# Kernel tuning notes

Measured on AMD Instinct MI355X. Metric: run time of the kernel, lower is better.

Reference implementation:

```python
import jax, jax.numpy as jnp
import numpy as np
import math

N_PTS = 262144
STEP_LENGTH = math.sqrt(3.0) / 1024.0  # step_length = sqrt(3)/steps


def pos_enc(x):
    # classic NeRF frequency encoding: identity + sin/cos at 10 octaves -> 3 + 3*2*10 = 63
    freqs = 2.0 ** jnp.arange(10, dtype=x.dtype)            # [10]
    xb = x[..., :, None] * freqs                            # [N,3,10]
    xb = xb.reshape(x.shape[0], -1)                         # [N,30]
    return jnp.concatenate([x, jnp.sin(xb), jnp.cos(xb)], axis=-1)  # [N,63]


def dir_enc(u):
    # 26-dim frequency encoding of (dir+1)/2 (color head input 283 = 256 + 26 + 1).
    # 13 sin/cos pairs: per-channel octaves 2^0..2^4, truncated to 13 frequencies.
    freqs = 2.0 ** jnp.arange(5, dtype=u.dtype)             # [5]
    z = (u[..., :, None] * freqs).reshape(u.shape[0], -1)[:, :13]  # [N,13]
    return jnp.concatenate([jnp.sin(z), jnp.cos(z)], axis=-1)      # [N,26]


def linear(x, w, b):
    return x @ w.T + b


def setup_inputs() -> dict:
    key = jax.random.key(0)
    ks = jax.random.split(key, 16)
    s = 0.05
    inp = {
        "position": jax.random.uniform(ks[0], (N_PTS, 3), dtype=jnp.float32),
        "direction": jax.random.uniform(ks[1], (N_PTS, 3), dtype=jnp.float32, minval=-1.0, maxval=1.0),
        "w1_in": jax.random.normal(ks[2], (256, 63), jnp.float32) * s,
        "b1_in": jnp.zeros((256,), jnp.float32),
        "w1_h": jax.random.normal(ks[3], (3, 256, 256), jnp.float32) * s,
        "b1_h": jnp.zeros((3, 256), jnp.float32),
        "w2_in": jax.random.normal(ks[4], (256, 319), jnp.float32) * s,
        "b2_in": jnp.zeros((256,), jnp.float32),
        "w2_h": jax.random.normal(ks[5], (3, 256, 256), jnp.float32) * s,
        "b2_h": jnp.zeros((3, 256), jnp.float32),
        # sigma head Linear(256,1)
        "w_sigma": jax.random.normal(ks[6], (1, 256), jnp.float32) * s,
        "b_sigma": jnp.zeros((1,), jnp.float32),
        # color head Linear(283,128) -> ReLU -> Linear(128,3)
        "w_c1": jax.random.normal(ks[7], (128, 283), jnp.float32) * s,
        "b_c1": jnp.zeros((128,), jnp.float32),
        "w_c2": jax.random.normal(ks[8], (3, 128), jnp.float32) * s,
        "b_c2": jnp.zeros((3,), jnp.float32),
    }
    return inp


def reference(position, direction,
              w1_in, b1_in, w1_h, b1_h,
              w2_in, b2_in, w2_h, b2_h,
              w_sigma, b_sigma, w_c1, b_c1, w_c2, b_c2):
    pe = pos_enc(position)                                  # [N,63]
    h = jax.nn.relu(linear(pe, w1_in, b1_in))               # [N,256]
    for i in range(3):
        h = jax.nn.relu(linear(h, w1_h[i], b1_h[i]))
    g = jax.nn.relu(linear(jnp.concatenate([h, pe], axis=-1), w2_in, b2_in))  # [N,256]
    for i in range(3):
        g = jax.nn.relu(linear(g, w2_h[i], b2_h[i]))
    sigma_raw = linear(g, w_sigma, b_sigma)                 # [N,1]
    # get_alpha: 1 - exp(-relu(sigma) * step_length)
    alphas = 1.0 - jnp.exp(-jax.nn.relu(sigma_raw) * STEP_LENGTH)             # [N,1]
    # get_rgb: shares base features; concat [256 | 26 | 1] = 283
    de = dir_enc((direction + 1.0) * 0.5)                   # [N,26]
    feats = jnp.concatenate([g, de, sigma_raw], axis=-1)    # [N,283]
    rgb = jax.nn.sigmoid(linear(jax.nn.relu(linear(feats, w_c1, b_c1)), w_c2, b_c2))  # [N,3]
    return (rgb, alphas)
```

## Files before the change

kernel.cpp:

```cpp
#include <hip/hip_runtime.h>
#include <hip/hip_bf16.h>

#define N_PTS 262144
#define STEP_LEN 0.0016914558667664818f

using f32x4 = __attribute__((ext_vector_type(4))) float;
using s8 = __attribute__((ext_vector_type(8))) short;

__device__ __forceinline__ float bf2f(short s) {
    union { unsigned int u; float f; } v;
    v.u = ((unsigned int)(unsigned short)s) << 16;
    return v.f;
}
__device__ __forceinline__ short f2bf(float f) {
    __hip_bfloat16 h = __float2bfloat16(f);
    return *reinterpret_cast<short*>(&h);
}

#define OFF_W1    0
#define OFF_L1H0  16384
#define OFF_W2    212992
#define OFF_L2H0  294912
#define OFF_C1G   491520
#define OFF_C1DE  524288
#define OFF_WSIG  528384
#define OFF_WC2   528640
#define WS_ELEMS  532480

__device__ __forceinline__ float hid_val(const float* __restrict__ W, int e) {
    int j = e & 7, lane = (e >> 3) & 63, nt = (e >> 9) & 15, ks = e >> 13;
    int n = nt * 16 + (lane & 15), hi = lane >> 4;
    int f = ks * 32 + ((j >> 2) << 4) + hi * 4 + (j & 3);
    return W[n * 256 + f];
}

__global__ void prep_weights(const float* __restrict__ w1_in,
                             const float* __restrict__ w1_h,
                             const float* __restrict__ w2_in,
                             const float* __restrict__ w2_h,
                             const float* __restrict__ w_c1,
                             const float* __restrict__ w_sigma,
                             const float* __restrict__ w_c2,
                             __hip_bfloat16* __restrict__ ws) {
    int i = blockIdx.x * blockDim.x + threadIdx.x;
    if (i >= WS_ELEMS) return;
    float v;
    if (i < OFF_L1H0) {
        int e = i;
        int j = e & 7, lane = (e >> 3) & 63, nt = (e >> 9) & 15, ks = e >> 13;
        int n = nt * 16 + (lane & 15), hi = lane >> 4;
        int f = ks * 32 + hi * 8 + j;
        v = (f < 63) ? w1_in[n * 63 + f] : 0.f;
    } else if (i < OFF_W2) {
        int e = i - OFF_L1H0; int sub = e >> 16; e &= 65535;
        v = hid_val(w1_h + sub * 65536, e);
    } else if (i < OFF_L2H0) {
        int e = i - OFF_W2;
        int j = e & 7, lane = (e >> 3) & 63, nt = (e >> 9) & 15, ks = e >> 13;
        int n = nt * 16 + (lane & 15), hi = lane >> 4;
        if (ks < 8) {
            int f = ks * 32 + ((j >> 2) << 4) + hi * 4 + (j & 3);
            v = w2_in[n * 319 + f];
        } else {
            int pf = (ks - 8) * 32 + hi * 8 + j;
            v = (pf < 63) ? w2_in[n * 319 + 256 + pf] : 0.f;
        }
    } else if (i < OFF_C1G) {
        int e = i - OFF_L2H0; int sub = e >> 16; e &= 65535;
        v = hid_val(w2_h + sub * 65536, e);
    } else if (i < OFF_C1DE) {
        int e = i - OFF_C1G;
        int j = e & 7, lane = (e >> 3) & 63, nt = (e >> 9) & 7, ks = e >> 12;
        int n = nt * 16 + (lane & 15), hi = lane >> 4;
        int f = ks * 32 + ((j >> 2) << 4) + hi * 4 + (j & 3);
        v = w_c1[n * 283 + f];
    } else if (i < OFF_WSIG) {
        int e = i - OFF_C1DE;
        int j = e & 7, lane = (e >> 3) & 63, nt = (e >> 9) & 7;
        int n = nt * 16 + (lane & 15), hi = lane >> 4;
        int k = 256 + hi * 8 + j;
        v = (k < 283) ? w_c1[n * 283 + k] : 0.f;
    } else if (i < OFF_WC2) {
        int e = i - OFF_WSIG;
        int j = e & 7, hi = (e >> 3) & 3, ks = e >> 5;
        int f = ks * 32 + ((j >> 2) << 4) + hi * 4 + (j & 3);
        v = w_sigma[f];
    } else if (i < 529024) {
        int e = i - OFF_WC2;
        int j = e & 7, hi = (e >> 3) & 3, ks = (e >> 5) & 3, ch = e >> 7;
        int f = ks * 32 + ((j >> 2) << 4) + hi * 4 + (j & 3);
        v = w_c2[ch * 128 + f];
    } else {
        v = 0.f;
    }
    ws[i] = __float2bfloat16(v);
}

__device__ __forceinline__ float enc3(int f, float x0, float x1, float x2) {
    if (f < 3) return (f == 0) ? x0 : ((f == 1) ? x1 : x2);
    if (f < 33) {
        int q = f - 3; int c = q / 10, o = q % 10;
        float xc = (c == 0) ? x0 : ((c == 1) ? x1 : x2);
        return __sinf(xc * (float)(1 << o));
    }
    if (f < 63) {
        int q = f - 33; int c = q / 10, o = q % 10;
        float xc = (c == 0) ? x0 : ((c == 1) ? x1 : x2);
        return __cosf(xc * (float)(1 << o));
    }
    return 0.f;
}

#define MFMA16 __builtin_amdgcn_mfma_f32_16x16x32_bf16

#define GLL(SRC, DST) __builtin_amdgcn_global_load_lds( \
    (const unsigned int*)(SRC), (unsigned int*)(DST), 16, 0, 0)

#define STAGE8(BYTEOFF, DBUF) do { \
    const char* _src = wsB + (long)(BYTEOFF) + wid * 8192 + lane * 16; \
    char* _dst = (DBUF) + wid * 8192; \
    GLL(_src,        _dst);        GLL(_src + 1024, _dst + 1024); \
    GLL(_src + 2048, _dst + 2048); GLL(_src + 3072, _dst + 3072); \
    GLL(_src + 4096, _dst + 4096); GLL(_src + 5120, _dst + 5120); \
    GLL(_src + 6144, _dst + 6144); GLL(_src + 7168, _dst + 7168); \
} while (0)

#define WHALF(RD, SUB, A0, A1, FIRSTV) do { \
    _Pragma("unroll") \
    for (int nt = 0; nt < 16; ++nt) { \
        const s8 w = *(const s8*)((RD) + (SUB) + nt * 1024 + lane * 16); \
        acc[nt][0] = MFMA16(w, (A0), (FIRSTV) ? Z : acc[nt][0], 0, 0, 0); \
        acc[nt][1] = MFMA16(w, (A1), (FIRSTV) ? Z : acc[nt][1], 0, 0, 0); \
    } } while (0)

#define CHALF(RD, SUB, A0, A1, FIRSTV) do { \
    _Pragma("unroll") \
    for (int nt = 0; nt < 8; ++nt) { \
        const s8 w = *(const s8*)((RD) + (SUB) + nt * 1024 + lane * 16); \
        acc[nt][0] = MFMA16(w, (A0), (FIRSTV) ? Z : acc[nt][0], 0, 0, 0); \
        acc[nt][1] = MFMA16(w, (A1), (FIRSTV) ? Z : acc[nt][1], 0, 0, 0); \
    } } while (0)

#define PBAR do { asm volatile("s_waitcnt vmcnt(0)" ::: "memory"); \
                  __builtin_amdgcn_s_barrier(); } while (0)

#define CONVERTL(BOFF) do { \
    _Pragma("unroll") \
    for (int nt = 0; nt < 16; ++nt) { \
        const f32x4 b4 = *(const f32x4*)(biasL + (((BOFF) + nt * 16 + hi4) << 2)); \
        _Pragma("unroll") \
        for (int r = 0; r < 4; ++r) { \
            actA[nt >> 1][((nt & 1) << 2) | r] = f2bf(fmaxf(acc[nt][0][r] + b4[r], 0.f)); \
            actB[nt >> 1][((nt & 1) << 2) | r] = f2bf(fmaxf(acc[nt][1][r] + b4[r], 0.f)); \
        } } } while (0)

#define LAYER4_ODD(CB, BO) do { \
    STAGE8((CB) +  32768, B0); __builtin_amdgcn_s_setprio(1); \
    WHALF(B1, 0, actA[0], actB[0], 1); WHALF(B1, 16384, actA[1], actB[1], 0); \
    __builtin_amdgcn_s_setprio(0); PBAR; \
    STAGE8((CB) +  65536, B1); __builtin_amdgcn_s_setprio(1); \
    WHALF(B0, 0, actA[2], actB[2], 0); WHALF(B0, 16384, actA[3], actB[3], 0); \
    __builtin_amdgcn_s_setprio(0); PBAR; \
    STAGE8((CB) +  98304, B0); __builtin_amdgcn_s_setprio(1); \
    WHALF(B1, 0, actA[4], actB[4], 0); WHALF(B1, 16384, actA[5], actB[5], 0); \
    __builtin_amdgcn_s_setprio(0); PBAR; \
    STAGE8((CB) + 131072, B1); __builtin_amdgcn_s_setprio(1); \
    WHALF(B0, 0, actA[6], actB[6], 0); WHALF(B0, 16384, actA[7], actB[7], 0); \
    __builtin_amdgcn_s_setprio(0); CONVERTL(BO); PBAR; \
} while (0)

#define LAYER4_EVEN(CB, BO) do { \
    STAGE8((CB) +  32768, B1); __builtin_amdgcn_s_setprio(1); \
    WHALF(B0, 0, actA[0], actB[0], 1); WHALF(B0, 16384, actA[1], actB[1], 0); \
    __builtin_amdgcn_s_setprio(0); PBAR; \
    STAGE8((CB) +  65536, B0); __builtin_amdgcn_s_setprio(1); \
    WHALF(B1, 0, actA[2], actB[2], 0); WHALF(B1, 16384, actA[3], actB[3], 0); \
    __builtin_amdgcn_s_setprio(0); PBAR; \
    STAGE8((CB) +  98304, B1); __builtin_amdgcn_s_setprio(1); \
    WHALF(B0, 0, actA[4], actB[4], 0); WHALF(B0, 16384, actA[5], actB[5], 0); \
    __builtin_amdgcn_s_setprio(0); PBAR; \
    STAGE8((CB) + 131072, B0); __builtin_amdgcn_s_setprio(1); \
    WHALF(B1, 0, actA[6], actB[6], 0); WHALF(B1, 16384, actA[7], actB[7], 0); \
    __builtin_amdgcn_s_setprio(0); CONVERTL(BO); PBAR; \
} while (0)

__global__ __launch_bounds__(256, 2) void nerf_fused(
    const float* __restrict__ pos, const float* __restrict__ dir,
    const __hip_bfloat16* __restrict__ ws,
    const float* __restrict__ b1_in, const float* __restrict__ b1_h,
    const float* __restrict__ b2_in, const float* __restrict__ b2_h,
    const float* __restrict__ b_sigma, const float* __restrict__ b_c1,
    const float* __restrict__ b_c2,
    float* __restrict__ out) {

    __shared__ __align__(16) char Lds[74240];
    char* const B0 = Lds;
    char* const B1 = Lds + 32768;
    char* const biasL = Lds + 65536;

    const int t = threadIdx.x;
    const int lane = t & 63;
    const int wid = t >> 6;
    const int hi = lane >> 4;
    const int col = lane & 15;
    const int hi4 = hi * 4;
    const int row0 = blockIdx.x * 128;
    const int gA = row0 + wid * 32 + col;
    const int gB = gA + 16;
    const char* wsB = (const char*)ws;

    STAGE8(0L, B0);

    for (int i = t; i < 2176; i += 256) {
        float v;
        if (i < 256) v = b1_in[i];
        else if (i < 1024) v = b1_h[i - 256];
        else if (i < 1280) v = b2_in[i - 1024];
        else if (i < 2048) v = b2_h[i - 1280];
        else v = b_c1[i - 2048];
        *(float*)(biasL + i * 4) = v;
    }

    s8 peA0, peA1, peB0, peB1;
    {
        float xa0 = pos[gA*3], xa1 = pos[gA*3+1], xa2 = pos[gA*3+2];
        float xb0 = pos[gB*3], xb1 = pos[gB*3+1], xb2 = pos[gB*3+2];
#pragma unroll
        for (int j = 0; j < 8; ++j) {
            int f0 = hi * 8 + j, f1 = 32 + hi * 8 + j;
            peA0[j] = f2bf(enc3(f0, xa0, xa1, xa2));
            peA1[j] = f2bf(enc3(f1, xa0, xa1, xa2));
            peB0[j] = f2bf(enc3(f0, xb0, xb1, xb2));
            peB1[j] = f2bf(enc3(f1, xb0, xb1, xb2));
        }
    }

    s8 deA, deB;
    {
        float uA0 = (dir[gA*3+0] + 1.f) * 0.5f;
        float uA1 = (dir[gA*3+1] + 1.f) * 0.5f;
        float uA2 = (dir[gA*3+2] + 1.f) * 0.5f;
        float uB0 = (dir[gB*3+0] + 1.f) * 0.5f;
        float uB1 = (dir[gB*3+1] + 1.f) * 0.5f;
        float uB2 = (dir[gB*3+2] + 1.f) * 0.5f;
#pragma unroll
        for (int j = 0; j < 8; ++j) {
            int d = hi * 8 + j;
            float vA = 0.f, vB = 0.f;
            if (d < 13) {
                int c = d / 5, o = d % 5; float s = (float)(1 << o);
                vA = __sinf(((c == 0) ? uA0 : (c == 1) ? uA1 : uA2) * s);
                vB = __sinf(((c == 0) ? uB0 : (c == 1) ? uB1 : uB2) * s);
            } else if (d < 26) {
                int q = d - 13; int c = q / 5, o = q % 5; float s = (float)(1 << o);
                vA = __cosf(((c == 0) ? uA0 : (c == 1) ? uA1 : uA2) * s);
                vB = __cosf(((c == 0) ? uB0 : (c == 1) ? uB1 : uB2) * s);
            }
            deA[j] = f2bf(vA); deB[j] = f2bf(vB);
        }
    }

    f32x4 acc[16][2];
    s8 actA[8], actB[8];
    const f32x4 Z = {0.f, 0.f, 0.f, 0.f};

    asm volatile("s_waitcnt vmcnt(0) lgkmcnt(0)" ::: "memory");
    __builtin_amdgcn_s_barrier();

    STAGE8(1L*32768, B1);
    __builtin_amdgcn_s_setprio(1);
    WHALF(B0, 0, peA0, peB0, 1); WHALF(B0, 16384, peA1, peB1, 0);
    __builtin_amdgcn_s_setprio(0);
    CONVERTL(0); PBAR;

#pragma unroll 1
    for (int l = 0; l < 3; ++l)
        LAYER4_ODD(32768L + (long)l * 131072, 256 + (l << 8));

    STAGE8(14L*32768, B0);
    __builtin_amdgcn_s_setprio(1);
    WHALF(B1, 0, actA[0], actB[0], 1); WHALF(B1, 16384, actA[1], actB[1], 0);
    __builtin_amdgcn_s_setprio(0); PBAR;
    STAGE8(15L*32768, B1);
    __builtin_amdgcn_s_setprio(1);
    WHALF(B0, 0, actA[2], actB[2], 0); WHALF(B0, 16384, actA[3], actB[3], 0);
    __builtin_amdgcn_s_setprio(0); PBAR;
    STAGE8(16L*32768, B0);
    __builtin_amdgcn_s_setprio(1);
    WHALF(B1, 0, actA[4], actB[4], 0); WHALF(B1, 16384, actA[5], actB[5], 0);
    __builtin_amdgcn_s_setprio(0); PBAR;
    STAGE8(17L*32768, B1);
    __builtin_amdgcn_s_setprio(1);
    WHALF(B0, 0, actA[6], actB[6], 0); WHALF(B0, 16384, actA[7], actB[7], 0);
    __builtin_amdgcn_s_setprio(0); PBAR;
    STAGE8(18L*32768, B0);
    __builtin_amdgcn_s_setprio(1);
    WHALF(B1, 0, peA0, peB0, 0); WHALF(B1, 16384, peA1, peB1, 0);
    __builtin_amdgcn_s_setprio(0);
    CONVERTL(1024); PBAR;

#pragma unroll 1
    for (int l = 0; l < 3; ++l)
        LAYER4_EVEN(589824L + (long)l * 131072, 1280 + (l << 8));

    float srA, srB, alphaA, alphaB;
    {
        float sA = 0.f, sB = 0.f;
#pragma unroll
        for (int ks = 0; ks < 8; ++ks) {
            const s8 wv = *(const s8*)(wsB + (OFF_WSIG + ks * 32 + hi * 8) * 2);
#pragma unroll
            for (int j = 0; j < 8; ++j) {
                sA += bf2f(actA[ks][j]) * bf2f(wv[j]);
                sB += bf2f(actB[ks][j]) * bf2f(wv[j]);
            }
        }
        sA += __shfl_xor(sA, 16); sA += __shfl_xor(sA, 32);
        sB += __shfl_xor(sB, 16); sB += __shfl_xor(sB, 32);
        srA = sA + b_sigma[0]; srB = sB + b_sigma[0];
        alphaA = 1.f - __expf(-fmaxf(srA, 0.f) * STEP_LEN);
        alphaB = 1.f - __expf(-fmaxf(srB, 0.f) * STEP_LEN);
        if (hi == 3) { deA[2] = f2bf(srA); deB[2] = f2bf(srB); }
    }

    STAGE8(31L*32768, B1);
    __builtin_amdgcn_s_setprio(1);
    CHALF(B0, 0,     actA[0], actB[0], 1);
    CHALF(B0, 8192,  actA[1], actB[1], 0);
    CHALF(B0, 16384, actA[2], actB[2], 0);
    CHALF(B0, 24576, actA[3], actB[3], 0);
    __builtin_amdgcn_s_setprio(0); PBAR;

    {
        const char* _src = wsB + 1048576L + wid * 2048 + lane * 16;
        char* _dst = B0 + wid * 2048;
        GLL(_src, _dst); GLL(_src + 1024, _dst + 1024);
    }
    __builtin_amdgcn_s_setprio(1);
    CHALF(B1, 0,     actA[4], actB[4], 0);
    CHALF(B1, 8192,  actA[5], actB[5], 0);
    CHALF(B1, 16384, actA[6], actB[6], 0);
    CHALF(B1, 24576, actA[7], actB[7], 0);
    __builtin_amdgcn_s_setprio(0); PBAR;

    __builtin_amdgcn_s_setprio(1);
#pragma unroll
    for (int nt = 0; nt < 8; ++nt) {
        const s8 w = *(const s8*)(B0 + nt * 1024 + lane * 16);
        acc[nt][0] = MFMA16(w, deA, acc[nt][0], 0, 0, 0);
        acc[nt][1] = MFMA16(w, deB, acc[nt][1], 0, 0, 0);
    }
    __builtin_amdgcn_s_setprio(0);

    s8 c1A[4], c1B[4];
#pragma unroll
    for (int nt = 0; nt < 8; ++nt) {
        const f32x4 b4 = *(const f32x4*)(biasL + ((2048 + nt * 16 + hi4) << 2));
#pragma unroll
        for (int r = 0; r < 4; ++r) {
            c1A[nt >> 1][((nt & 1) << 2) | r] = f2bf(fmaxf(acc[nt][0][r] + b4[r], 0.f));
            c1B[nt >> 1][((nt & 1) << 2) | r] = f2bf(fmaxf(acc[nt][1][r] + b4[r], 0.f));
        }
    }

#pragma unroll
    for (int ch = 0; ch < 3; ++ch) {
        float rA = 0.f, rB = 0.f;
#pragma unroll
        for (int ks = 0; ks < 4; ++ks) {
            const s8 wv = *(const s8*)(wsB + (OFF_WC2 + (ch * 4 + ks) * 32 + hi * 8) * 2);
#pragma unroll
            for (int j = 0; j < 8; ++j) {
                rA += bf2f(c1A[ks][j]) * bf2f(wv[j]);
                rB += bf2f(c1B[ks][j]) * bf2f(wv[j]);
            }
        }
        rA += __shfl_xor(rA, 16); rA += __shfl_xor(rA, 32);
        rB += __shfl_xor(rB, 16); rB += __shfl_xor(rB, 32);
        if (hi == 0) {
            out[gA * 3 + ch] = 1.f / (1.f + __expf(-(rA + b_c2[ch])));
            out[gB * 3 + ch] = 1.f / (1.f + __expf(-(rB + b_c2[ch])));
        }
    }
    if (hi == 0) {
        out[3 * N_PTS + gA] = alphaA;
        out[3 * N_PTS + gB] = alphaB;
    }
}

extern "C" void kernel_launch(void* const* d_in, const int* in_sizes, int n_in,
                              void* d_out, int out_size, void* d_ws, size_t ws_size,
                              hipStream_t stream) {
    const float* position = (const float*)d_in[0];
    const float* direction = (const float*)d_in[1];
    const float* w1_in = (const float*)d_in[2];
    const float* b1_in = (const float*)d_in[3];
    const float* w1_h  = (const float*)d_in[4];
    const float* b1_h  = (const float*)d_in[5];
    const float* w2_in = (const float*)d_in[6];
    const float* b2_in = (const float*)d_in[7];
    const float* w2_h  = (const float*)d_in[8];
    const float* b2_h  = (const float*)d_in[9];
    const float* w_sigma = (const float*)d_in[10];
    const float* b_sigma = (const float*)d_in[11];
    const float* w_c1  = (const float*)d_in[12];
    const float* b_c1  = (const float*)d_in[13];
    const float* w_c2  = (const float*)d_in[14];
    const float* b_c2  = (const float*)d_in[15];
    float* out = (float*)d_out;
    __hip_bfloat16* ws = (__hip_bfloat16*)d_ws;

    prep_weights<<<(WS_ELEMS + 255) / 256, 256, 0, stream>>>(
        w1_in, w1_h, w2_in, w2_h, w_c1, w_sigma, w_c2, ws);

    nerf_fused<<<N_PTS / 128, 256, 0, stream>>>(
        position, direction, ws,
        b1_in, b1_h, b2_in, b2_h,
        b_sigma, b_c1, b_c2, out);
}
```

Baseline: 243.3 us.

## Switch fused NeRF MLP from 16x16x32 to 32x32x16 bf16 MFMA tiles

Replaces the 16x16x32 MFMA instructions (two 16-row point tiles per wave) with 32x32x16 MFMA covering all 32 points per wave in one tile. The weight pre-packing layout, activation register layout, bias/ReLU conversion and the sigma and color-head reductions are all rewritten to match. The larger tile halves the number of MFMA issues and LDS weight reads per point. The layer loops are also fully unrolled via a LAYER4 macro. It relies on the new packed layouts and lane mappings being exactly consistent, and the 16-wide accumulators may raise register pressure.

```diff
diff --git a/kernel.cpp b/kernel.cpp
--- a/kernel.cpp
+++ b/kernel.cpp
@@ -5,6 +5,7 @@
 #define STEP_LEN 0.0016914558667664818f
 
 using f32x4 = __attribute__((ext_vector_type(4))) float;
+using f32x16 = __attribute__((ext_vector_type(16))) float;
 using s8 = __attribute__((ext_vector_type(8))) short;
 
 __device__ __forceinline__ float bf2f(short s) {
@@ -26,13 +27,6 @@
 #define OFF_WSIG  528384
 #define OFF_WC2   528640
 #define WS_ELEMS  532480
-
-__device__ __forceinline__ float hid_val(const float* __restrict__ W, int e) {
-    int j = e & 7, lane = (e >> 3) & 63, nt = (e >> 9) & 15, ks = e >> 13;
-    int n = nt * 16 + (lane & 15), hi = lane >> 4;
-    int f = ks * 32 + ((j >> 2) << 4) + hi * 4 + (j & 3);
-    return W[n * 256 + f];
-}
 
 __global__ void prep_weights(const float* __restrict__ w1_in,
                              const float* __restrict__ w1_h,
@@ -47,49 +41,55 @@
     float v;
     if (i < OFF_L1H0) {
         int e = i;
-        int j = e & 7, lane = (e >> 3) & 63, nt = (e >> 9) & 15, ks = e >> 13;
-        int n = nt * 16 + (lane & 15), hi = lane >> 4;
-        int f = ks * 32 + hi * 8 + j;
+        int j = e & 7, lane = (e >> 3) & 63, nt = (e >> 9) & 7, kc = e >> 12;
+        int n = nt * 32 + (lane & 31), h = lane >> 5;
+        int f = kc * 16 + h * 8 + j;
         v = (f < 63) ? w1_in[n * 63 + f] : 0.f;
     } else if (i < OFF_W2) {
         int e = i - OFF_L1H0; int sub = e >> 16; e &= 65535;
-        v = hid_val(w1_h + sub * 65536, e);
+        int j = e & 7, lane = (e >> 3) & 63, nt = (e >> 9) & 7, kc = e >> 12;
+        int n = nt * 32 + (lane & 31), h = lane >> 5;
+        int f = kc * 16 + ((j >> 2) << 3) + h * 4 + (j & 3);
+        v = w1_h[sub * 65536 + n * 256 + f];
     } else if (i < OFF_L2H0) {
         int e = i - OFF_W2;
-        int j = e & 7, lane = (e >> 3) & 63, nt = (e >> 9) & 15, ks = e >> 13;
-        int n = nt * 16 + (lane & 15), hi = lane >> 4;
-        if (ks < 8) {
-            int f = ks * 32 + ((j >> 2) << 4) + hi * 4 + (j & 3);
+        int j = e & 7, lane = (e >> 3) & 63, nt = (e >> 9) & 7, kc = e >> 12;
+        int n = nt * 32 + (lane & 31), h = lane >> 5;
+        if (kc < 16) {
+            int f = kc * 16 + ((j >> 2) << 3) + h * 4 + (j & 3);
             v = w2_in[n * 319 + f];
         } else {
-            int pf = (ks - 8) * 32 + hi * 8 + j;
+            int pf = (kc - 16) * 16 + h * 8 + j;
             v = (pf < 63) ? w2_in[n * 319 + 256 + pf] : 0.f;
         }
     } else if (i < OFF_C1G) {
         int e = i - OFF_L2H0; int sub = e >> 16; e &= 65535;
-        v = hid_val(w2_h + sub * 65536, e);
+        int j = e & 7, lane = (e >> 3) & 63, nt = (e >> 9) & 7, kc = e >> 12;
+        int n = nt * 32 + (lane & 31), h = lane >> 5;
+        int f = kc * 16 + ((j >> 2) << 3) + h * 4 + (j & 3);
+        v = w2_h[sub * 65536 + n * 256 + f];
     } else if (i < OFF_C1DE) {
         int e = i - OFF_C1G;
-        int j = e & 7, lane = (e >> 3) & 63, nt = (e >> 9) & 7, ks = e >> 12;
-        int n = nt * 16 + (lane & 15), hi = lane >> 4;
-        int f = ks * 32 + ((j >> 2) << 4) + hi * 4 + (j & 3);
+        int j = e & 7, lane = (e >> 3) & 63, nt = (e >> 9) & 3, kc = e >> 11;
+        int n = nt * 32 + (lane & 31), h = lane >> 5;
+        int f = kc * 16 + ((j >> 2) << 3) + h * 4 + (j & 3);
         v = w_c1[n * 283 + f];
     } else if (i < OFF_WSIG) {
         int e = i - OFF_C1DE;
-        int j = e & 7, lane = (e >> 3) & 63, nt = (e >> 9) & 7;
-        int n = nt * 16 + (lane & 15), hi = lane >> 4;
-        int k = 256 + hi * 8 + j;
+        int j = e & 7, lane = (e >> 3) & 63, nt = (e >> 9) & 3, kc = e >> 11;
+        int n = nt * 32 + (lane & 31), h = lane >> 5;
+        int k = 256 + kc * 16 + h * 8 + j;
         v = (k < 283) ? w_c1[n * 283 + k] : 0.f;
     } else if (i < OFF_WC2) {
         int e = i - OFF_WSIG;
-        int j = e & 7, hi = (e >> 3) & 3, ks = e >> 5;
-        int f = ks * 32 + ((j >> 2) << 4) + hi * 4 + (j & 3);
+        int j = e & 7, h = (e >> 3) & 1, kc = e >> 4;
+        int f = kc * 16 + ((j >> 2) << 3) + h * 4 + (j & 3);
         v = w_sigma[f];
     } else if (i < 529024) {
         int e = i - OFF_WC2;
-        int j = e & 7, hi = (e >> 3) & 3, ks = (e >> 5) & 3, ch = e >> 7;
-        int f = ks * 32 + ((j >> 2) << 4) + hi * 4 + (j & 3);
-        v = w_c2[ch * 128 + f];
+        int r = e & 15, h = (e >> 4) & 1, nt = (e >> 5) & 3, ch = e >> 7;
+        int n = nt * 32 + (r & 3) + 8 * (r >> 2) + 4 * h;
+        v = w_c2[ch * 128 + n];
     } else {
         v = 0.f;
     }
@@ -111,7 +111,7 @@
     return 0.f;
 }
 
-#define MFMA16 __builtin_amdgcn_mfma_f32_16x16x32_bf16
+#define MFMA32 __builtin_amdgcn_mfma_f32_32x32x16_bf16
 
 #define GLL(SRC, DST) __builtin_amdgcn_global_load_lds( \
     (const unsigned int*)(SRC), (unsigned int*)(DST), 16, 0, 0)
@@ -125,63 +125,60 @@
     GLL(_src + 6144, _dst + 6144); GLL(_src + 7168, _dst + 7168); \
 } while (0)
 
-#define WHALF(RD, SUB, A0, A1, FIRSTV) do { \
+#define SP1 __builtin_amdgcn_s_setprio(1)
+#define SP0 __builtin_amdgcn_s_setprio(0)
+
+#define WPAIR_A(RD, KC, FIRSTV) do { \
     _Pragma("unroll") \
-    for (int nt = 0; nt < 16; ++nt) { \
-        const s8 w = *(const s8*)((RD) + (SUB) + nt * 1024 + lane * 16); \
-        acc[nt][0] = MFMA16(w, (A0), (FIRSTV) ? Z : acc[nt][0], 0, 0, 0); \
-        acc[nt][1] = MFMA16(w, (A1), (FIRSTV) ? Z : acc[nt][1], 0, 0, 0); \
-    } } while (0)
-
-#define CHALF(RD, SUB, A0, A1, FIRSTV) do { \
+    for (int kc2 = 0; kc2 < 4; ++kc2) { \
+        _Pragma("unroll") \
+        for (int nt = 0; nt < 8; ++nt) { \
+            const s8 w = *(const s8*)((RD) + (kc2 * 8 + nt) * 1024 + lane * 16); \
+            acc[nt] = MFMA32(w, act[(KC) + kc2], \
+                             ((FIRSTV) && kc2 == 0) ? Z : acc[nt], 0, 0, 0); \
+        } } } while (0)
+
+#define WPAIR_P(RD, FIRSTV) do { \
+    _Pragma("unroll") \
+    for (int kc2 = 0; kc2 < 4; ++kc2) { \
+        _Pragma("unroll") \
+        for (int nt = 0; nt < 8; ++nt) { \
+            const s8 w = *(const s8*)((RD) + (kc2 * 8 + nt) * 1024 + lane * 16); \
+            acc[nt] = MFMA32(w, pe[kc2], \
+                             ((FIRSTV) && kc2 == 0) ? Z : acc[nt], 0, 0, 0); \
+        } } } while (0)
+
+#define CPAIR(RD, KC, FIRSTV) do { \
+    _Pragma("unroll") \
+    for (int kc2 = 0; kc2 < 8; ++kc2) { \
+        _Pragma("unroll") \
+        for (int nt = 0; nt < 4; ++nt) { \
+            const s8 w = *(const s8*)((RD) + (kc2 * 4 + nt) * 1024 + lane * 16); \
+            acc[nt] = MFMA32(w, act[(KC) + kc2], \
+                             ((FIRSTV) && kc2 == 0) ? Z : acc[nt], 0, 0, 0); \
+        } } } while (0)
+
+#define PBAR do { asm volatile("s_waitcnt vmcnt(0)" ::: "memory"); \
+                  __builtin_amdgcn_s_barrier(); } while (0)
+
+#define CONVERTL(BOFF) do { \
     _Pragma("unroll") \
     for (int nt = 0; nt < 8; ++nt) { \
-        const s8 w = *(const s8*)((RD) + (SUB) + nt * 1024 + lane * 16); \
-        acc[nt][0] = MFMA16(w, (A0), (FIRSTV) ? Z : acc[nt][0], 0, 0, 0); \
-        acc[nt][1] = MFMA16(w, (A1), (FIRSTV) ? Z : acc[nt][1], 0, 0, 0); \
-    } } while (0)
-
-#define PBAR do { asm volatile("s_waitcnt vmcnt(0)" ::: "memory"); \
-                  __builtin_amdgcn_s_barrier(); } while (0)
-
-#define CONVERTL(BOFF) do { \
-    _Pragma("unroll") \
-    for (int nt = 0; nt < 16; ++nt) { \
-        const f32x4 b4 = *(const f32x4*)(biasL + (((BOFF) + nt * 16 + hi4) << 2)); \
         _Pragma("unroll") \
-        for (int r = 0; r < 4; ++r) { \
-            actA[nt >> 1][((nt & 1) << 2) | r] = f2bf(fmaxf(acc[nt][0][r] + b4[r], 0.f)); \
-            actB[nt >> 1][((nt & 1) << 2) | r] = f2bf(fmaxf(acc[nt][1][r] + b4[r], 0.f)); \
-        } } } while (0)
-
-#define LAYER4_ODD(CB, BO) do { \
-    STAGE8((CB) +  32768, B0); __builtin_amdgcn_s_setprio(1); \
-    WHALF(B1, 0, actA[0], actB[0], 1); WHALF(B1, 16384, actA[1], actB[1], 0); \
-    __builtin_amdgcn_s_setprio(0); PBAR; \
-    STAGE8((CB) +  65536, B1); __builtin_amdgcn_s_setprio(1); \
-    WHALF(B0, 0, actA[2], actB[2], 0); WHALF(B0, 16384, actA[3], actB[3], 0); \
-    __builtin_amdgcn_s_setprio(0); PBAR; \
-    STAGE8((CB) +  98304, B0); __builtin_amdgcn_s_setprio(1); \
-    WHALF(B1, 0, actA[4], actB[4], 0); WHALF(B1, 16384, actA[5], actB[5], 0); \
-    __builtin_amdgcn_s_setprio(0); PBAR; \
-    STAGE8((CB) + 131072, B1); __builtin_amdgcn_s_setprio(1); \
-    WHALF(B0, 0, actA[6], actB[6], 0); WHALF(B0, 16384, actA[7], actB[7], 0); \
-    __builtin_amdgcn_s_setprio(0); CONVERTL(BO); PBAR; \
-} while (0)
-
-#define LAYER4_EVEN(CB, BO) do { \
-    STAGE8((CB) +  32768, B1); __builtin_amdgcn_s_setprio(1); \
-    WHALF(B0, 0, actA[0], actB[0], 1); WHALF(B0, 16384, actA[1], actB[1], 0); \
-    __builtin_amdgcn_s_setprio(0); PBAR; \
-    STAGE8((CB) +  65536, B0); __builtin_amdgcn_s_setprio(1); \
-    WHALF(B1, 0, actA[2], actB[2], 0); WHALF(B1, 16384, actA[3], actB[3], 0); \
-    __builtin_amdgcn_s_setprio(0); PBAR; \
-    STAGE8((CB) +  98304, B1); __builtin_amdgcn_s_setprio(1); \
-    WHALF(B0, 0, actA[4], actB[4], 0); WHALF(B0, 16384, actA[5], actB[5], 0); \
-    __builtin_amdgcn_s_setprio(0); PBAR; \
-    STAGE8((CB) + 131072, B0); __builtin_amdgcn_s_setprio(1); \
-    WHALF(B1, 0, actA[6], actB[6], 0); WHALF(B1, 16384, actA[7], actB[7], 0); \
-    __builtin_amdgcn_s_setprio(0); CONVERTL(BO); PBAR; \
+        for (int q = 0; q < 4; ++q) { \
+            const f32x4 b4 = *(const f32x4*)(biasL + (((BOFF) + nt * 32 + q * 8 + h4) << 2)); \
+            _Pragma("unroll") \
+            for (int i2 = 0; i2 < 4; ++i2) { \
+                float x = fmaxf(acc[nt][q * 4 + i2] + b4[i2], 0.f); \
+                act[nt * 2 + (q >> 1)][((q & 1) << 2) | i2] = f2bf(x); \
+            } } } } while (0)
+
+#define LAYER4(P, X, Y, BO) do { \
+    STAGE8((long)((P) + 1) * 32768, Y); SP1; WPAIR_A(X, 0, 1);  SP0; PBAR; \
+    STAGE8((long)((P) + 2) * 32768, X); SP1; WPAIR_A(Y, 4, 0);  SP0; PBAR; \
+    STAGE8((long)((P) + 3) * 32768, Y); SP1; WPAIR_A(X, 8, 0);  SP0; PBAR; \
+    STAGE8((long)((P) + 4) * 32768, X); SP1; WPAIR_A(Y, 12, 0); SP0; \
+    CONVERTL(BO); PBAR; \
 } while (0)
 
 __global__ __launch_bounds__(256, 2) void nerf_fused(
@@ -201,12 +198,12 @@
     const int t = threadIdx.x;
     const int lane = t & 63;
     const int wid = t >> 6;
-    const int hi = lane >> 4;
-    const int col = lane & 15;
-    const int hi4 = hi * 4;
+    const int h = lane >> 5;
+    const int h4 = h * 4;
+    const int h8 = h * 8;
+    const int h16 = h * 16;
     const int row0 = blockIdx.x * 128;
-    const int gA = row0 + wid * 32 + col;
-    const int gB = gA + 16;
+    const int g = row0 + wid * 32 + (lane & 31);
     const char* wsB = (const char*)ws;
 
     STAGE8(0L, B0);
@@ -221,170 +218,133 @@
         *(float*)(biasL + i * 4) = v;
     }
 
-    s8 peA0, peA1, peB0, peB1;
+    s8 pe[4];
     {
-        float xa0 = pos[gA*3], xa1 = pos[gA*3+1], xa2 = pos[gA*3+2];
-        float xb0 = pos[gB*3], xb1 = pos[gB*3+1], xb2 = pos[gB*3+2];
-#pragma unroll
-        for (int j = 0; j < 8; ++j) {
-            int f0 = hi * 8 + j, f1 = 32 + hi * 8 + j;
-            peA0[j] = f2bf(enc3(f0, xa0, xa1, xa2));
-            peA1[j] = f2bf(enc3(f1, xa0, xa1, xa2));
-            peB0[j] = f2bf(enc3(f0, xb0, xb1, xb2));
-            peB1[j] = f2bf(enc3(f1, xb0, xb1, xb2));
-        }
-    }
-
-    s8 deA, deB;
+        float x0 = pos[g * 3], x1 = pos[g * 3 + 1], x2 = pos[g * 3 + 2];
+#pragma unroll
+        for (int kc = 0; kc < 4; ++kc)
+#pragma unroll
+            for (int j = 0; j < 8; ++j)
+                pe[kc][j] = f2bf(enc3(kc * 16 + h8 + j, x0, x1, x2));
+    }
+
+    s8 de[2];
     {
-        float uA0 = (dir[gA*3+0] + 1.f) * 0.5f;
-        float uA1 = (dir[gA*3+1] + 1.f) * 0.5f;
-        float uA2 = (dir[gA*3+2] + 1.f) * 0.5f;
-        float uB0 = (dir[gB*3+0] + 1.f) * 0.5f;
-        float uB1 = (dir[gB*3+1] + 1.f) * 0.5f;
-        float uB2 = (dir[gB*3+2] + 1.f) * 0.5f;
-#pragma unroll
-        for (int j = 0; j < 8; ++j) {
-            int d = hi * 8 + j;
-            float vA = 0.f, vB = 0.f;
-            if (d < 13) {
-                int c = d / 5, o = d % 5; float s = (float)(1 << o);
-                vA = __sinf(((c == 0) ? uA0 : (c == 1) ? uA1 : uA2) * s);
-                vB = __sinf(((c == 0) ? uB0 : (c == 1) ? uB1 : uB2) * s);
-            } else if (d < 26) {
-                int q = d - 13; int c = q / 5, o = q % 5; float s = (float)(1 << o);
-                vA = __cosf(((c == 0) ? uA0 : (c == 1) ? uA1 : uA2) * s);
-                vB = __cosf(((c == 0) ? uB0 : (c == 1) ? uB1 : uB2) * s);
+        float u0 = (dir[g * 3 + 0] + 1.f) * 0.5f;
+        float u1 = (dir[g * 3 + 1] + 1.f) * 0.5f;
+        float u2 = (dir[g * 3 + 2] + 1.f) * 0.5f;
+#pragma unroll
+        for (int dc = 0; dc < 2; ++dc)
+#pragma unroll
+            for (int j = 0; j < 8; ++j) {
+                int d = dc * 16 + h8 + j;
+                float v = 0.f;
+                if (d < 13) {
+                    int c = d / 5, o = d % 5;
+                    v = __sinf(((c == 0) ? u0 : (c == 1) ? u1 : u2) * (float)(1 << o));
+                } else if (d < 26) {
+                    int q = d - 13; int c = q / 5, o = q % 5;
+                    v = __cosf(((c == 0) ? u0 : (c == 1) ? u1 : u2) * (float)(1 << o));
+                }
+                de[dc][j] = f2bf(v);
             }
-            deA[j] = f2bf(vA); deB[j] = f2bf(vB);
-        }
-    }
-
-    f32x4 acc[16][2];
-    s8 actA[8], actB[8];
-    const f32x4 Z = {0.f, 0.f, 0.f, 0.f};
+    }
+
+    f32x16 acc[8];
+    s8 act[16];
+    const f32x16 Z = {0.f, 0.f, 0.f, 0.f, 0.f, 0.f, 0.f, 0.f,
+                      0.f, 0.f, 0.f, 0.f, 0.f, 0.f, 0.f, 0.f};
 
     asm volatile("s_waitcnt vmcnt(0) lgkmcnt(0)" ::: "memory");
     __builtin_amdgcn_s_barrier();
 
-    STAGE8(1L*32768, B1);
-    __builtin_amdgcn_s_setprio(1);
-    WHALF(B0, 0, peA0, peB0, 1); WHALF(B0, 16384, peA1, peB1, 0);
-    __builtin_amdgcn_s_setprio(0);
+    STAGE8(1L * 32768, B1);
+    SP1; WPAIR_P(B0, 1); SP0;
     CONVERTL(0); PBAR;
 
-#pragma unroll 1
-    for (int l = 0; l < 3; ++l)
-        LAYER4_ODD(32768L + (long)l * 131072, 256 + (l << 8));
-
-    STAGE8(14L*32768, B0);
-    __builtin_amdgcn_s_setprio(1);
-    WHALF(B1, 0, actA[0], actB[0], 1); WHALF(B1, 16384, actA[1], actB[1], 0);
-    __builtin_amdgcn_s_setprio(0); PBAR;
-    STAGE8(15L*32768, B1);
-    __builtin_amdgcn_s_setprio(1);
-    WHALF(B0, 0, actA[2], actB[2], 0); WHALF(B0, 16384, actA[3], actB[3], 0);
-    __builtin_amdgcn_s_setprio(0); PBAR;
-    STAGE8(16L*32768, B0);
-    __builtin_amdgcn_s_setprio(1);
-    WHALF(B1, 0, actA[4], actB[4], 0); WHALF(B1, 16384, actA[5], actB[5], 0);
-    __builtin_amdgcn_s_setprio(0); PBAR;
-    STAGE8(17L*32768, B1);
-    __builtin_amdgcn_s_setprio(1);
-    WHALF(B0, 0, actA[6], actB[6], 0); WHALF(B0, 16384, actA[7], actB[7], 0);
-    __builtin_amdgcn_s_setprio(0); PBAR;
-    STAGE8(18L*32768, B0);
-    __builtin_amdgcn_s_setprio(1);
-    WHALF(B1, 0, peA0, peB0, 0); WHALF(B1, 16384, peA1, peB1, 0);
-    __builtin_amdgcn_s_setprio(0);
+    LAYER4(1, B1, B0, 256);
+    LAYER4(5, B1, B0, 512);
+    LAYER4(9, B1, B0, 768);
+
+    STAGE8(14L * 32768, B0); SP1; WPAIR_A(B1, 0, 1);  SP0; PBAR;
+    STAGE8(15L * 32768, B1); SP1; WPAIR_A(B0, 4, 0);  SP0; PBAR;
+    STAGE8(16L * 32768, B0); SP1; WPAIR_A(B1, 8, 0);  SP0; PBAR;
+    STAGE8(17L * 32768, B1); SP1; WPAIR_A(B0, 12, 0); SP0; PBAR;
+    STAGE8(18L * 32768, B0); SP1; WPAIR_P(B1, 0);     SP0;
     CONVERTL(1024); PBAR;
 
-#pragma unroll 1
-    for (int l = 0; l < 3; ++l)
-        LAYER4_EVEN(589824L + (long)l * 131072, 1280 + (l << 8));
-
-    float srA, srB, alphaA, alphaB;
+    LAYER4(18, B0, B1, 1280);
+    LAYER4(22, B0, B1, 1536);
+    LAYER4(26, B0, B1, 1792);
+
+    STAGE8(31L * 32768, B1);
+    float sr, alpha;
     {
-        float sA = 0.f, sB = 0.f;
-#pragma unroll
-        for (int ks = 0; ks < 8; ++ks) {
-            const s8 wv = *(const s8*)(wsB + (OFF_WSIG + ks * 32 + hi * 8) * 2);
-#pragma unroll
-            for (int j = 0; j < 8; ++j) {
-                sA += bf2f(actA[ks][j]) * bf2f(wv[j]);
-                sB += bf2f(actB[ks][j]) * bf2f(wv[j]);
-            }
-        }
-        sA += __shfl_xor(sA, 16); sA += __shfl_xor(sA, 32);
-        sB += __shfl_xor(sB, 16); sB += __shfl_xor(sB, 32);
-        srA = sA + b_sigma[0]; srB = sB + b_sigma[0];
-        alphaA = 1.f - __expf(-fmaxf(srA, 0.f) * STEP_LEN);
-        alphaB = 1.f - __expf(-fmaxf(srB, 0.f) * STEP_LEN);
-        if (hi == 3) { deA[2] = f2bf(srA); deB[2] = f2bf(srB); }
-    }
-
-    STAGE8(31L*32768, B1);
-    __builtin_amdgcn_s_setprio(1);
-    CHALF(B0, 0,     actA[0], actB[0], 1);
-    CHALF(B0, 8192,  actA[1], actB[1], 0);
-    CHALF(B0, 16384, actA[2], actB[2], 0);
-    CHALF(B0, 24576, actA[3], actB[3], 0);
-    __builtin_amdgcn_s_setprio(0); PBAR;
+        float s = 0.f;
+#pragma unroll
+        for (int kc = 0; kc < 16; ++kc) {
+            const s8 wv = *(const s8*)(wsB + (OFF_WSIG + kc * 16 + h8) * 2);
+#pragma unroll
+            for (int j = 0; j < 8; ++j)
+                s += bf2f(act[kc][j]) * bf2f(wv[j]);
+        }
+        s += __shfl_xor(s, 32);
+        sr = s + b_sigma[0];
+        alpha = 1.f - __expf(-fmaxf(sr, 0.f) * STEP_LEN);
+        if (lane >= 32) de[1][2] = f2bf(sr);
+    }
+    SP1; CPAIR(B0, 0, 1); SP0; PBAR;
 
     {
         const char* _src = wsB + 1048576L + wid * 2048 + lane * 16;
         char* _dst = B0 + wid * 2048;
         GLL(_src, _dst); GLL(_src + 1024, _dst + 1024);
     }
-    __builtin_amdgcn_s_setprio(1);
-    CHALF(B1, 0,     actA[4], actB[4], 0);
-    CHALF(B1, 8192,  actA[5], actB[5], 0);
-    CHALF(B1, 16384, actA[6], actB[6], 0);
-    CHALF(B1, 24576, actA[7], actB[7], 0);
-    __builtin_amdgcn_s_setprio(0); PBAR;
-
-    __builtin_amdgcn_s_setprio(1);
-#pragma unroll
-    for (int nt = 0; nt < 8; ++nt) {
-        const s8 w = *(const s8*)(B0 + nt * 1024 + lane * 16);
-        acc[nt][0] = MFMA16(w, deA, acc[nt][0], 0, 0, 0);
-        acc[nt][1] = MFMA16(w, deB, acc[nt][1], 0, 0, 0);
-    }
-    __builtin_amdgcn_s_setprio(0);
-
-    s8 c1A[4], c1B[4];
-#pragma unroll
-    for (int nt = 0; nt < 8; ++nt) {
-        const f32x4 b4 = *(const f32x4*)(biasL + ((2048 + nt * 16 + hi4) << 2));
-#pragma unroll
-        for (int r = 0; r < 4; ++r) {
-            c1A[nt >> 1][((nt & 1) << 2) | r] = f2bf(fmaxf(acc[nt][0][r] + b4[r], 0.f));
-            c1B[nt >> 1][((nt & 1) << 2) | r] = f2bf(fmaxf(acc[nt][1][r] + b4[r], 0.f));
-        }
-    }
-
-#pragma unroll
-    for (int ch = 0; ch < 3; ++ch) {
-        float rA = 0.f, rB = 0.f;
-#pragma unroll
-        for (int ks = 0; ks < 4; ++ks) {
-            const s8 wv = *(const s8*)(wsB + (OFF_WC2 + (ch * 4 + ks) * 32 + hi * 8) * 2);
-#pragma unroll
-            for (int j = 0; j < 8; ++j) {
-                rA += bf2f(c1A[ks][j]) * bf2f(wv[j]);
-                rB += bf2f(c1B[ks][j]) * bf2f(wv[j]);
-            }
-        }
-        rA += __shfl_xor(rA, 16); rA += __shfl_xor(rA, 32);
-        rB += __shfl_xor(rB, 16); rB += __shfl_xor(rB, 32);
-        if (hi == 0) {
-            out[gA * 3 + ch] = 1.f / (1.f + __expf(-(rA + b_c2[ch])));
-            out[gB * 3 + ch] = 1.f / (1.f + __expf(-(rB + b_c2[ch])));
-        }
-    }
-    if (hi == 0) {
-        out[3 * N_PTS + gA] = alphaA;
-        out[3 * N_PTS + gB] = alphaB;
+    SP1; CPAIR(B1, 8, 0); SP0; PBAR;
+
+    SP1;
+#pragma unroll
+    for (int kc2 = 0; kc2 < 2; ++kc2)
+#pragma unroll
+        for (int nt = 0; nt < 4; ++nt) {
+            const s8 w = *(const s8*)(B0 + (kc2 * 4 + nt) * 1024 + lane * 16);
+            acc[nt] = MFMA32(w, de[kc2], acc[nt], 0, 0, 0);
+        }
+    SP0;
+
+    float rr0 = 0.f, rr1 = 0.f, rr2 = 0.f;
+#pragma unroll
+    for (int nt = 0; nt < 4; ++nt) {
+        float c1v[16];
+#pragma unroll
+        for (int q = 0; q < 4; ++q) {
+            const f32x4 b4 = *(const f32x4*)(biasL + ((2048 + nt * 32 + q * 8 + h4) << 2));
+#pragma unroll
+            for (int i2 = 0; i2 < 4; ++i2)
+                c1v[q * 4 + i2] = fmaxf(acc[nt][q * 4 + i2] + b4[i2], 0.f);
+        }
+        const long wb = (long)(OFF_WC2 + nt * 32 + h16) * 2;
+        const s8 w0a = *(const s8*)(wsB + wb);
+        const s8 w0b = *(const s8*)(wsB + wb + 16);
+        const s8 w1a = *(const s8*)(wsB + wb + 256);
+        const s8 w1b = *(const s8*)(wsB + wb + 272);
+        const s8 w2a = *(const s8*)(wsB + wb + 512);
+        const s8 w2b = *(const s8*)(wsB + wb + 528);
+#pragma unroll
+        for (int r = 0; r < 8; ++r) {
+            rr0 += c1v[r] * bf2f(w0a[r]) + c1v[8 + r] * bf2f(w0b[r]);
+            rr1 += c1v[r] * bf2f(w1a[r]) + c1v[8 + r] * bf2f(w1b[r]);
+            rr2 += c1v[r] * bf2f(w2a[r]) + c1v[8 + r] * bf2f(w2b[r]);
+        }
+    }
+    rr0 += __shfl_xor(rr0, 32);
+    rr1 += __shfl_xor(rr1, 32);
+    rr2 += __shfl_xor(rr2, 32);
+    if (lane < 32) {
+        out[g * 3 + 0] = 1.f / (1.f + __expf(-(rr0 + b_c2[0])));
+        out[g * 3 + 1] = 1.f / (1.f + __expf(-(rr1 + b_c2[1])));
+        out[g * 3 + 2] = 1.f / (1.f + __expf(-(rr2 + b_c2[2])));
+        out[3 * N_PTS + g] = alpha;
     }
 }
 
```

Result: slower. 258.9 us (+6.4%).
